# Optimization experiments

Measured on AMD Instinct MI355X. Metric: run time of the kernel, lower is better.

Reference implementation:

```python
import math
import jax, jax.numpy as jnp
import numpy as np

B, C, H, W = 8, 128, 128, 128

def _cosine_basis(n):
    pos = (jnp.arange(n, dtype=jnp.float32) + 0.5) / n          # [n]
    freq = jnp.arange(n, dtype=jnp.float32)[:, None]            # [n,1]
    basis = jnp.cos(freq * pos[None, :] * math.pi) * math.sqrt(2.0 / n)
    return basis.at[0, :].multiply(1.0 / math.sqrt(2.0))        # [n,n]


def setup_inputs() -> dict:
    key = jax.random.key(0)
    ks = jax.random.split(key, 12)
    s = 0.02
    return {
        "x":        jax.random.normal(ks[0], (B, C, H, W), jnp.float32),
        "dw_w":     jax.random.normal(ks[1], (C, 1, 3, 3), jnp.float32) * s,
        "dw_b":     jnp.zeros((C,), jnp.float32),
        "in_w":     jax.random.normal(ks[2], (2 * C, C), jnp.float32) * s,
        "in_b":     jnp.zeros((2 * C,), jnp.float32),
        "out_w":    jax.random.normal(ks[3], (C, C), jnp.float32) * s,
        "out_b":    jnp.zeros((C,), jnp.float32),
        "ln_w":     jnp.ones((C,), jnp.float32),
        "ln_b":     jnp.zeros((C,), jnp.float32),
        "ph_w":     jax.random.normal(ks[4], (C, C), jnp.float32) * s,
        "ph_b":     jnp.zeros((C,), jnp.float32),
        "wave_speed": jnp.ones((1,), jnp.float32),
        "damping":    jnp.full((1,), 0.1, jnp.float32),
        "freq_embed": jax.random.normal(ks[5], (H, W, C), jnp.float32) * s,
    }


def reference(x, dw_w, dw_b, in_w, in_b, out_w, out_b, ln_w, ln_b,
              ph_w, ph_b, wave_speed, damping, freq_embed):
    # depthwise 3x3 conv (groups=C), padding=1
    mixed = jax.lax.conv_general_dilated(
        x, dw_w, window_strides=(1, 1), padding=((1, 1), (1, 1)),
        dimension_numbers=("NCHW", "OIHW", "NCHW"), feature_group_count=C)
    mixed = mixed + dw_b[None, :, None, None]
    mixed = jnp.transpose(mixed, (0, 2, 3, 1))                  # [B,H,W,C]

    proj = mixed @ in_w.T + in_b                                # [B,H,W,2C]
    carrier, gate = jnp.split(proj, 2, axis=-1)

    cos_h = _cosine_basis(H)
    cos_w = _cosine_basis(W)
    # DCT-II along H then W
    spectral = jnp.einsum("bhwc,nh->bnwc", carrier, cos_h)
    spectral = jnp.einsum("bnwc,mw->bnmc", spectral, cos_w)     # [B,H,W,C] (freq)

    # phase modulation (base_resolution == H == W, so no resize)
    phase = jax.nn.gelu(freq_embed @ ph_w.T + ph_b, approximate=False)  # [H,W,C]
    wave_phase = wave_speed * phase                             # broadcast [H,W,C]
    vel_scale = jnp.sin(wave_phase) / jnp.maximum(jnp.abs(wave_speed), 1e-6)
    modulated = (jnp.cos(wave_phase) + vel_scale * (1.0 + 0.5 * damping)) * spectral

    # inverse DCT
    fused = jnp.einsum("bnmc,wm->bnwc", modulated, cos_w.T)
    fused = jnp.einsum("bnwc,hn->bhwc", fused, cos_h.T)         # [B,H,W,C]

    # LayerNorm over channels
    mu = jnp.mean(fused, axis=-1, keepdims=True)
    var = jnp.mean(jnp.square(fused - mu), axis=-1, keepdims=True)
    fused = (fused - mu) / jnp.sqrt(var + 1e-5) * ln_w + ln_b

    fused = fused * jax.nn.silu(gate)
    out = fused @ out_w.T + out_b                               # [B,H,W,C]
    return jnp.transpose(out, (0, 3, 1, 2))                     # [B,C,H,W]
```

## Files before the change

### kernel.cpp

```cpp
#include <hip/hip_runtime.h>
#include <math.h>

#ifndef M_PI
#define M_PI 3.14159265358979323846
#endif

typedef float fx4 __attribute__((ext_vector_type(4)));
typedef __bf16 bf16x8 __attribute__((ext_vector_type(8)));
typedef __bf16 bf16x4 __attribute__((ext_vector_type(4)));

__device__ __forceinline__ unsigned short f2bf(float f){
  union { float f; unsigned u; } v; v.f = f;
  unsigned r = v.u + 0x7FFFu + ((v.u >> 16) & 1u);
  return (unsigned short)(r >> 16);
}
__device__ __forceinline__ float bf2f(unsigned short u){
  union { unsigned u; float f; } v; v.u = ((unsigned)u) << 16;
  return v.f;
}
__device__ __forceinline__ int swz(int row, int colbyte){
  return row*256 + (colbyte ^ ((row & 7) << 4));
}

template<typename FA, typename FB>
__device__ __forceinline__ void run_gemm(FA la, FB lb, fx4 (&acc)[4][4]){
  bf16x8 a[2][4], b[2][4];
  #pragma unroll
  for (int mi=0;mi<4;mi++){ a[0][mi]=la(mi,0); b[0][mi]=lb(mi,0); }
  #pragma unroll
  for (int ks=0; ks<4; ks++){
    int cur = ks&1, nxt = cur^1;
    if (ks<3){
      #pragma unroll
      for (int mi=0;mi<4;mi++){ a[nxt][mi]=la(mi,ks+1); b[nxt][mi]=lb(mi,ks+1); }
    }
    #pragma unroll
    for (int mi=0;mi<4;mi++)
      #pragma unroll
      for (int ni=0;ni<4;ni++)
        acc[mi][ni] = __builtin_amdgcn_mfma_f32_16x16x32_bf16(a[cur][mi], b[cur][ni], acc[mi][ni], 0, 0, 0);
  }
}

template<typename FA0, typename FA1, typename FB>
__device__ __forceinline__ void run_pair_sharedB(FA0 la0, FA1 la1, FB lb,
                                                 fx4 (&acc0)[4][4], fx4 (&acc1)[4][4]){
  bf16x8 a0[2][4], a1[2][4], b[2][4];
  #pragma unroll
  for (int mi=0;mi<4;mi++){ a0[0][mi]=la0(mi,0); a1[0][mi]=la1(mi,0); b[0][mi]=lb(mi,0); }
  #pragma unroll
  for (int ks=0; ks<4; ks++){
    int cur = ks&1, nxt = cur^1;
    if (ks<3){
      #pragma unroll
      for (int mi=0;mi<4;mi++){ a0[nxt][mi]=la0(mi,ks+1); a1[nxt][mi]=la1(mi,ks+1); b[nxt][mi]=lb(mi,ks+1); }
    }
    #pragma unroll
    for (int mi=0;mi<4;mi++)
      #pragma unroll
      for (int ni=0;ni<4;ni++){
        acc0[mi][ni] = __builtin_amdgcn_mfma_f32_16x16x32_bf16(a0[cur][mi], b[cur][ni], acc0[mi][ni], 0, 0, 0);
        acc1[mi][ni] = __builtin_amdgcn_mfma_f32_16x16x32_bf16(a1[cur][mi], b[cur][ni], acc1[mi][ni], 0, 0, 0);
      }
  }
}

template<typename FA, typename FB0, typename FB1>
__device__ __forceinline__ void run_pair_sharedA(FA la, FB0 lb0, FB1 lb1,
                                                 fx4 (&acc0)[4][4], fx4 (&acc1)[4][4]){
  bf16x8 a[2][4], b0[2][4], b1[2][4];
  #pragma unroll
  for (int mi=0;mi<4;mi++){ a[0][mi]=la(mi,0); b0[0][mi]=lb0(mi,0); b1[0][mi]=lb1(mi,0); }
  #pragma unroll
  for (int ks=0; ks<4; ks++){
    int cur = ks&1, nxt = cur^1;
    if (ks<3){
      #pragma unroll
      for (int mi=0;mi<4;mi++){ a[nxt][mi]=la(mi,ks+1); b0[nxt][mi]=lb0(mi,ks+1); b1[nxt][mi]=lb1(mi,ks+1); }
    }
    #pragma unroll
    for (int mi=0;mi<4;mi++)
      #pragma unroll
      for (int ni=0;ni<4;ni++){
        acc0[mi][ni] = __builtin_amdgcn_mfma_f32_16x16x32_bf16(a[cur][mi], b0[cur][ni], acc0[mi][ni], 0, 0, 0);
        acc1[mi][ni] = __builtin_amdgcn_mfma_f32_16x16x32_bf16(a[cur][mi], b1[cur][ni], acc1[mi][ni], 0, 0, 0);
      }
  }
}

__global__ __launch_bounds__(256) void k1_prep_cast_conv(
    const float* __restrict__ in_w, const float* __restrict__ ph_w,
    const float* __restrict__ out_w, const float* __restrict__ fe,
    const float* __restrict__ x, const float* __restrict__ dw_w,
    const float* __restrict__ dw_b,
    unsigned short* __restrict__ basis_bf, unsigned short* __restrict__ basisT_bf,
    unsigned short* __restrict__ ph_w_bf, unsigned short* __restrict__ in_w_bf,
    unsigned short* __restrict__ out_w_bf, unsigned short* __restrict__ feb,
    unsigned short* __restrict__ conv)
{
  int blk = blockIdx.x;
  int t = threadIdx.x;
  if (blk < 128){
    if (t >= 128) return;
    int n = blk, h = t;
    double arg = (double)(n*(2*h+1)) * (M_PI/256.0);
    double v = cos(arg) * 0.125;
    if (n==0) v *= 0.7071067811865476;
    unsigned short bv = f2bf((float)v);
    basis_bf[n*128+h]  = bv;
    basisT_bf[h*128+n] = bv;
    ph_w_bf[n*128+h]  = f2bf(ph_w[n*128+h]);
    in_w_bf[n*128+h]        = f2bf(in_w[n*128+h]);
    in_w_bf[(n+128)*128+h]  = f2bf(in_w[(n+128)*128+h]);
    out_w_bf[n*128+h]       = f2bf(out_w[n*128+h]);
    return;
  }
  if (blk < 1152){
    int idx = (blk-128)*256 + t;
    const float* s = fe + (size_t)idx*8;
    float4 f0 = *(const float4*)s;
    float4 f1 = *(const float4*)(s+4);
    unsigned short o[8];
    o[0]=f2bf(f0.x); o[1]=f2bf(f0.y); o[2]=f2bf(f0.z); o[3]=f2bf(f0.w);
    o[4]=f2bf(f1.x); o[5]=f2bf(f1.y); o[6]=f2bf(f1.z); o[7]=f2bf(f1.w);
    *(int4*)(feb + (size_t)idx*8) = *(const int4*)o;
    return;
  }
  {
    int bb = blk - 1152;
    int plane = bb >> 2, band = bb & 3;
    int c = plane & 127;
    const float* xp = x + (size_t)plane*16384;
    unsigned short* op = conv + (size_t)plane*16384;
    const float* kw = dw_w + c*9;
    float k0=kw[0],k1=kw[1],k2=kw[2],k3=kw[3],k4=kw[4],k5=kw[5],k6=kw[6],k7=kw[7],k8=kw[8];
    float bias = dw_b[c];
    int q = t & 31;
    int w0 = q*4;
    int rg = t >> 5;
    int h0 = band*32 + rg*4;
    bool le = (q==0), re = (q==31);
    float4 fA, fB, fC; float lA,rA,lB,rB,lC,rC;
    #define LOADROW(hh, f, l, r) { \
      int hc = (hh)<0 ? 0 : ((hh)>127 ? 127 : (hh)); \
      f = *(const float4*)(xp + hc*128 + w0); \
      float lu = __shfl_up(f.w, 1, 32); \
      float rd = __shfl_down(f.x, 1, 32); \
      l = le ? 0.f : lu; \
      r = re ? 0.f : rd; \
      if ((hh)<0 || (hh)>127){ f = make_float4(0.f,0.f,0.f,0.f); l=0.f; r=0.f; } \
    }
    LOADROW(h0-1, fA,lA,rA);
    LOADROW(h0,   fB,lB,rB);
    #pragma unroll
    for (int i=0;i<4;i++){
      LOADROW(h0+1+i, fC,lC,rC);
      float4 o;
      o.x = bias; o.y = bias; o.z = bias; o.w = bias;
      o.x = fmaf(k0,lA,  fmaf(k1,fA.x, fmaf(k2,fA.y, o.x)));
      o.y = fmaf(k0,fA.x,fmaf(k1,fA.y, fmaf(k2,fA.z, o.y)));
      o.z = fmaf(k0,fA.y,fmaf(k1,fA.z, fmaf(k2,fA.w, o.z)));
      o.w = fmaf(k0,fA.z,fmaf(k1,fA.w, fmaf(k2,rA,   o.w)));
      o.x = fmaf(k3,lB,  fmaf(k4,fB.x, fmaf(k5,fB.y, o.x)));
      o.y = fmaf(k3,fB.x,fmaf(k4,fB.y, fmaf(k5,fB.z, o.y)));
      o.z = fmaf(k3,fB.y,fmaf(k4,fB.z, fmaf(k5,fB.w, o.z)));
      o.w = fmaf(k3,fB.z,fmaf(k4,fB.w, fmaf(k5,rB,   o.w)));
      o.x = fmaf(k6,lC,  fmaf(k7,fC.x, fmaf(k8,fC.y, o.x)));
      o.y = fmaf(k6,fC.x,fmaf(k7,fC.y, fmaf(k8,fC.z, o.y)));
      o.z = fmaf(k6,fC.y,fmaf(k7,fC.z, fmaf(k8,fC.w, o.z)));
      o.w = fmaf(k6,fC.z,fmaf(k7,fC.w, fmaf(k8,rC,   o.w)));
      bf16x4 v;
      v[0]=(__bf16)o.x; v[1]=(__bf16)o.y; v[2]=(__bf16)o.z; v[3]=(__bf16)o.w;
      *(bf16x4*)(op + (size_t)(h0+i)*128 + w0) = v;
      fA=fB; lA=lB; rA=rB;
      fB=fC; lB=lC; rB=rC;
    }
    #undef LOADROW
  }
}

__global__ __launch_bounds__(512) void k2_inproj_projk(
  const unsigned short* __restrict__ conv, const unsigned short* __restrict__ in_w_bf,
  const float* __restrict__ in_b, unsigned short* __restrict__ carrier,
  unsigned short* __restrict__ gate,
  const unsigned short* __restrict__ feb, const unsigned short* __restrict__ ph_w_bf,
  float* __restrict__ projT)
{
  int blk = blockIdx.x;
  int t = threadIdx.x;
  if (blk >= 1024){
    if (t >= 256) return;
    int r0 = (blk - 1024) * 128;
    int l = t & 63, wid = t >> 6;
    int wm = wid >> 1, wn = wid & 1;
    int lr = l & 15, lk = (l>>4)*8, ld4 = (l>>4)*4;
    fx4 acc[4][4];
    #pragma unroll
    for (int i=0;i<4;i++) for (int j=0;j<4;j++) acc[i][j] = (fx4){0.f,0.f,0.f,0.f};
    run_gemm(
      [&](int mi,int ks)->bf16x8{ return *(const bf16x8*)(feb + (size_t)(r0 + wm*64+mi*16+lr)*128 + ks*32+lk); },
      [&](int ni,int ks)->bf16x8{ return *(const bf16x8*)(ph_w_bf + (size_t)(wn*64+ni*16+lr)*128 + ks*32+lk); },
      acc);
    #pragma unroll
    for (int mi=0;mi<4;mi++)
      #pragma unroll
      for (int ni=0;ni<4;ni++){
        int c = wn*64 + ni*16 + lr;
        int r = r0 + wm*64 + mi*16 + ld4;
        *(fx4*)(projT + (size_t)c*16384 + r) = acc[mi][ni];
      }
    return;
  }
  __shared__ char A[32768];
  int b = blk>>7, h = blk&127;
  const unsigned short* C = conv + (size_t)b*2097152 + h*128;
  {
    int wl = t & 63, grp = t >> 6;
    #pragma unroll
    for (int p=0;p<2;p++){
      int w = wl + 64*p;
      #pragma unroll
      for (int q=0;q<4;q++){
        int c0 = (q*8 + grp)*4;
        ushort4 v;
        v.x = C[(size_t)(c0+0)*16384 + w];
        v.y = C[(size_t)(c0+1)*16384 + w];
        v.z = C[(size_t)(c0+2)*16384 + w];
        v.w = C[(size_t)(c0+3)*16384 + w];
        *(ushort4*)(A + swz(w, c0*2)) = v;
      }
    }
  }
  __syncthreads();
  int l = t & 63, wid = t >> 6;
  int wm = wid >> 2, wn = wid & 3;
  int lr = l & 15, lk = (l>>4)*8, ld4 = (l>>4)*4;
  fx4 acc[4][4];
  #pragma unroll
  for (int i=0;i<4;i++) for (int j=0;j<4;j++) acc[i][j] = (fx4){0.f,0.f,0.f,0.f};
  run_gemm(
    [&](int mi,int ks)->bf16x8{ return *(const bf16x8*)(A + swz(wm*64+mi*16+lr, (ks*32+lk)*2)); },
    [&](int ni,int ks)->bf16x8{ return *(const bf16x8*)(in_w_bf + (size_t)(wn*64+ni*16+lr)*128 + ks*32+lk); },
    acc);
  __syncthreads();
  if (wn < 2){
    #pragma unroll
    for (int mi=0;mi<4;mi++)
      #pragma unroll
      for (int ni=0;ni<4;ni++){
        int n = wn*64 + ni*16 + lr;
        int w0 = wm*64 + mi*16 + ld4;
        float bias = in_b[n];
        ushort4 v;
        v.x=f2bf(acc[mi][ni][0]+bias); v.y=f2bf(acc[mi][ni][1]+bias);
        v.z=f2bf(acc[mi][ni][2]+bias); v.w=f2bf(acc[mi][ni][3]+bias);
        *(ushort4*)(carrier + (size_t)(b*128+n)*16384 + h*128 + w0) = v;
      }
  } else {
    #pragma unroll
    for (int mi=0;mi<4;mi++)
      #pragma unroll
      for (int ni=0;ni<4;ni++){
        int n = wn*64 + ni*16 + lr;
        int c = n - 128;
        int w0 = wm*64 + mi*16 + ld4;
        float bias = in_b[n];
        #pragma unroll
        for (int r=0;r<4;r++){
          float v = acc[mi][ni][r] + bias;
          float s = v / (1.0f + __expf(-v));
          *(unsigned short*)(A + swz(w0+r, c*2)) = f2bf(s);
        }
      }
  }
  __syncthreads();
  {
    unsigned short* gout = gate + ((size_t)(b*128+h))*16384;
    int w = t >> 2, cq = (t & 3) * 32;
    #pragma unroll
    for (int i=0;i<4;i++){
      int c0 = cq + i*8;
      int4 v = *(const int4*)(A + swz(w, c0*2));
      *(int4*)(gout + w*128 + c0) = v;
    }
  }
}

__global__ __launch_bounds__(256) void modfin_kernel(
  const float* __restrict__ projT, const float* __restrict__ ph_b,
  const float* __restrict__ wave_speed, const float* __restrict__ damping,
  float* __restrict__ modT)
{
  int blk = blockIdx.x;
  int c = blk >> 4, qb = blk & 15;
  int t = threadIdx.x;
  int q = qb*8 + (t>>5);
  int p0 = (t & 31)*4;
  float ws0 = wave_speed[0];
  float dmp = damping[0];
  float inv = 1.0f / fmaxf(fabsf(ws0), 1e-6f);
  float dampf = 1.0f + 0.5f*dmp;
  float bc = ph_b[c];
  const float* src = projT + (size_t)c*16384 + q;
  float o[4];
  #pragma unroll
  for (int i=0;i<4;i++){
    float v = src[(size_t)(p0+i)*128] + bc;
    float g = 0.5f*v*(1.0f + erff(v*0.70710678118f));
    float wp = ws0*g;
    o[i] = __cosf(wp) + __sinf(wp)*inv*dampf;
  }
  *(float4*)(modT + ((size_t)c*128 + q)*128 + p0) = make_float4(o[0],o[1],o[2],o[3]);
}

__global__ __launch_bounds__(256) void wave_kernel(
  const unsigned short* __restrict__ carrier,
  const unsigned short* __restrict__ basis,
  const unsigned short* __restrict__ basisT,
  const float* __restrict__ modT,
  unsigned short* __restrict__ fused)
{
  __shared__ char U0[32768];
  __shared__ char U1[32768];
  int blk = blockIdx.x;
  int c = blk & 127;
  const unsigned short* X0 = carrier + (size_t)blk*16384;
  const unsigned short* X1 = carrier + (size_t)(blk+512)*16384;
  unsigned short* F0 = fused + (size_t)blk*16384;
  unsigned short* F1 = fused + (size_t)(blk+512)*16384;
  int t = threadIdx.x;
  int l = t & 63, wid = t >> 6;
  int wm = wid >> 1, wn = wid & 1;
  int lr = l & 15, lk = (l>>4)*8, ld4 = (l>>4)*4;
  fx4 acc0[4][4], acc1[4][4];

  #define ZACC { _Pragma("unroll") for (int i=0;i<4;i++) _Pragma("unroll") for (int j=0;j<4;j++){ acc0[i][j]=(fx4){0.f,0.f,0.f,0.f}; acc1[i][j]=(fx4){0.f,0.f,0.f,0.f}; } }
  #define TSTORE(BUF0, BUF1) { \
    _Pragma("unroll") for (int mi=0;mi<4;mi++) \
      _Pragma("unroll") for (int ni=0;ni<4;ni++){ \
        int rr = wn*64 + ni*16 + lr, cc = wm*64 + mi*16 + ld4; \
        bf16x4 v0, v1; \
        v0[0]=(__bf16)acc0[mi][ni][0]; v0[1]=(__bf16)acc0[mi][ni][1]; \
        v0[2]=(__bf16)acc0[mi][ni][2]; v0[3]=(__bf16)acc0[mi][ni][3]; \
        v1[0]=(__bf16)acc1[mi][ni][0]; v1[1]=(__bf16)acc1[mi][ni][1]; \
        v1[2]=(__bf16)acc1[mi][ni][2]; v1[3]=(__bf16)acc1[mi][ni][3]; \
        *(bf16x4*)(BUF0 + swz(rr, cc*2)) = v0; \
        *(bf16x4*)(BUF1 + swz(rr, cc*2)) = v1; \
      } }

  ZACC;
  run_pair_sharedB(
    [&](int mi,int ks)->bf16x8{ return *(const bf16x8*)(X0 + (size_t)(wm*64+mi*16+lr)*128 + ks*32+lk); },
    [&](int mi,int ks)->bf16x8{ return *(const bf16x8*)(X1 + (size_t)(wm*64+mi*16+lr)*128 + ks*32+lk); },
    [&](int ni,int ks)->bf16x8{ return *(const bf16x8*)(basis + (size_t)(wn*64+ni*16+lr)*128 + ks*32+lk); },
    acc0, acc1);
  TSTORE(U0, U1);
  __syncthreads();

  ZACC;
  run_pair_sharedA(
    [&](int mi,int ks)->bf16x8{ return *(const bf16x8*)(basis + (size_t)(wm*64+mi*16+lr)*128 + ks*32+lk); },
    [&](int ni,int ks)->bf16x8{ return *(const bf16x8*)(U0 + swz(wn*64+ni*16+lr, (ks*32+lk)*2)); },
    [&](int ni,int ks)->bf16x8{ return *(const bf16x8*)(U1 + swz(wn*64+ni*16+lr, (ks*32+lk)*2)); },
    acc0, acc1);
  {
    const float* Mc = modT + (size_t)c*16384;
    #pragma unroll
    for (int mi=0;mi<4;mi++)
      #pragma unroll
      for (int ni=0;ni<4;ni++){
        int n0 = wm*64 + mi*16 + ld4, m = wn*64 + ni*16 + lr;
        fx4 mv = *(const fx4*)(Mc + (size_t)m*128 + n0);
        acc0[mi][ni] *= mv;
        acc1[mi][ni] *= mv;
      }
  }
  __syncthreads();
  TSTORE(U0, U1);
  __syncthreads();

  ZACC;
  run_pair_sharedB(
    [&](int mi,int ks)->bf16x8{ return *(const bf16x8*)(U0 + swz(wm*64+mi*16+lr, (ks*32+lk)*2)); },
    [&](int mi,int ks)->bf16x8{ return *(const bf16x8*)(U1 + swz(wm*64+mi*16+lr, (ks*32+lk)*2)); },
    [&](int ni,int ks)->bf16x8{ return *(const bf16x8*)(basisT + (size_t)(wn*64+ni*16+lr)*128 + ks*32+lk); },
    acc0, acc1);
  __syncthreads();
  TSTORE(U0, U1);
  __syncthreads();

  ZACC;
  run_pair_sharedA(
    [&](int mi,int ks)->bf16x8{ return *(const bf16x8*)(basisT + (size_t)(wm*64+mi*16+lr)*128 + ks*32+lk); },
    [&](int ni,int ks)->bf16x8{ return *(const bf16x8*)(U0 + swz(wn*64+ni*16+lr, (ks*32+lk)*2)); },
    [&](int ni,int ks)->bf16x8{ return *(const bf16x8*)(U1 + swz(wn*64+ni*16+lr, (ks*32+lk)*2)); },
    acc0, acc1);
  #pragma unroll
  for (int mi=0;mi<4;mi++)
    #pragma unroll
    for (int ni=0;ni<4;ni++){
      int hh = wn*64 + ni*16 + lr, w0 = wm*64 + mi*16 + ld4;
      bf16x4 v0, v1;
      v0[0]=(__bf16)acc0[mi][ni][0]; v0[1]=(__bf16)acc0[mi][ni][1];
      v0[2]=(__bf16)acc0[mi][ni][2]; v0[3]=(__bf16)acc0[mi][ni][3];
      v1[0]=(__bf16)acc1[mi][ni][0]; v1[1]=(__bf16)acc1[mi][ni][1];
      v1[2]=(__bf16)acc1[mi][ni][2]; v1[3]=(__bf16)acc1[mi][ni][3];
      *(bf16x4*)(F0 + hh*128 + w0) = v0;
      *(bf16x4*)(F1 + hh*128 + w0) = v1;
    }
  #undef ZACC
  #undef TSTORE
}

__global__ __launch_bounds__(256) void final_kernel(
  const unsigned short* __restrict__ fused, const unsigned short* __restrict__ gate,
  const unsigned short* __restrict__ out_w_bf, const float* __restrict__ out_b,
  const float* __restrict__ ln_w, const float* __restrict__ ln_b,
  float* __restrict__ out)
{
  __shared__ char Fl[32768];
  __shared__ char Al[32768];
  __shared__ float red[256], red2[256];
  __shared__ float mu[128], rs[128];
  int blk = blockIdx.x; int b = blk>>7, h = blk&127;
  const unsigned short* Fsrc = fused + (size_t)b*2097152 + h*128;
  const unsigned short* G = gate + (size_t)blk*16384;
  int t = threadIdx.x;
  {
    int c = t>>1, wq = (t&1)*64;
    #pragma unroll
    for (int i=0;i<8;i++){
      int w0 = wq + i*8;
      int4 v = *(const int4*)(Fsrc + (size_t)c*16384 + w0);
      *(int4*)(Fl + swz(c, w0*2)) = v;
    }
  }
  __syncthreads();
  {
    int w = t&127, half = t>>7;
    float s=0.f, q=0.f;
    for (int i=0;i<64;i++){
      int c = half*64 + i;
      float f = bf2f(*(const unsigned short*)(Fl + swz(c, w*2)));
      s += f; q = fmaf(f,f,q);
    }
    red[t]=s; red2[t]=q;
  }
  __syncthreads();
  if (t < 128){
    float ss = red[t]+red[t+128], qq = red2[t]+red2[t+128];
    float m = ss*(1.f/128.f);
    float var = qq*(1.f/128.f) - m*m;
    mu[t]=m; rs[t]=rsqrtf(var+1e-5f);
  }
  __syncthreads();
  {
    int w = t>>1, cq = (t&1)*64;
    float m_ = mu[w], r_ = rs[w];
    #pragma unroll
    for (int i=0;i<8;i++){
      int c0 = cq + i*8;
      ushort4 g0 = *(const ushort4*)(G + (size_t)w*128 + c0);
      ushort4 g1 = *(const ushort4*)(G + (size_t)w*128 + c0 + 4);
      unsigned short ov[8];
      unsigned short gv[8] = {g0.x,g0.y,g0.z,g0.w,g1.x,g1.y,g1.z,g1.w};
      #pragma unroll
      for (int j=0;j<8;j++){
        int cc = c0+j;
        float f = bf2f(*(const unsigned short*)(Fl + swz(cc, w*2)));
        float a = fmaf((f-m_)*r_, ln_w[cc], ln_b[cc]) * bf2f(gv[j]);
        ov[j] = f2bf(a);
      }
      *(int4*)(Al + swz(w, c0*2)) = *(const int4*)ov;
    }
  }
  __syncthreads();
  int l = t & 63, wid = t >> 6;
  int wm = wid >> 1, wn = wid & 1;
  int lr = l & 15, lk = (l>>4)*8, ld4 = (l>>4)*4;
  fx4 acc[4][4];
  #pragma unroll
  for (int i=0;i<4;i++) for (int j=0;j<4;j++) acc[i][j] = (fx4){0.f,0.f,0.f,0.f};
  run_gemm(
    [&](int mi,int ks)->bf16x8{ return *(const bf16x8*)(Al + swz(wm*64+mi*16+lr, (ks*32+lk)*2)); },
    [&](int ni,int ks)->bf16x8{ return *(const bf16x8*)(out_w_bf + (size_t)(wn*64+ni*16+lr)*128 + ks*32+lk); },
    acc);
  #pragma unroll
  for (int mi=0;mi<4;mi++)
    #pragma unroll
    for (int ni=0;ni<4;ni++){
      int j = wn*64 + ni*16 + lr, w0 = wm*64 + mi*16 + ld4;
      float bj = out_b[j];
      fx4 o = acc[mi][ni];
      o[0]+=bj; o[1]+=bj; o[2]+=bj; o[3]+=bj;
      *(fx4*)(out + ((size_t)(b*128 + j)*128 + h)*128 + w0) = o;
    }
}

extern "C" void kernel_launch(void* const* d_in, const int* in_sizes, int n_in,
                              void* d_out, int out_size, void* d_ws, size_t ws_size,
                              hipStream_t stream)
{
  const float* x      = (const float*)d_in[0];
  const float* dw_w   = (const float*)d_in[1];
  const float* dw_b   = (const float*)d_in[2];
  const float* in_w   = (const float*)d_in[3];
  const float* in_b   = (const float*)d_in[4];
  const float* out_w  = (const float*)d_in[5];
  const float* out_b  = (const float*)d_in[6];
  const float* ln_w   = (const float*)d_in[7];
  const float* ln_b   = (const float*)d_in[8];
  const float* ph_w   = (const float*)d_in[9];
  const float* ph_b   = (const float*)d_in[10];
  const float* wsp    = (const float*)d_in[11];
  const float* dmp    = (const float*)d_in[12];
  const float* fe     = (const float*)d_in[13];
  float* outp = (float*)d_out;

  float* modT  = (float*)d_ws;
  float* projT = modT + 2097152;
  unsigned short* feb      = (unsigned short*)(projT + 2097152);
  unsigned short* conv     = feb     + 2097152;
  unsigned short* carrier  = conv    + 16777216;
  unsigned short* gate     = carrier + 16777216;
  unsigned short* fusedb   = gate    + 16777216;
  unsigned short* basis_bf = fusedb  + 16777216;
  unsigned short* basisT_bf= basis_bf + 16384;
  unsigned short* in_w_bf  = basisT_bf + 16384;
  unsigned short* out_w_bf = in_w_bf + 32768;
  unsigned short* ph_w_bf  = out_w_bf + 16384;

  k1_prep_cast_conv<<<5248,256,0,stream>>>(in_w, ph_w, out_w, fe, x, dw_w, dw_b,
      basis_bf, basisT_bf, ph_w_bf, in_w_bf, out_w_bf, feb, conv);
  k2_inproj_projk<<<1152,512,0,stream>>>(conv, in_w_bf, in_b, carrier, gate,
      feb, ph_w_bf, projT);
  modfin_kernel<<<2048,256,0,stream>>>(projT, ph_b, wsp, dmp, modT);
  wave_kernel<<<512,256,0,stream>>>(carrier, basis_bf, basisT_bf, modT, fusedb);
  final_kernel<<<1024,256,0,stream>>>(fusedb, gate, out_w_bf, out_b, ln_w, ln_b, outp);
}
```

Baseline: 156.3 us.

## Fuse depthwise conv into in-projection kernel, drop conv intermediate buffer

Moves the depthwise 3x3 convolution from the prep kernel into the in-projection GEMM kernel, computing each (b,h) row's conv output directly into shared memory. This removes the bf16 conv intermediate write and its strided re-read from global memory. In exchange each block reads three input rows per channel (halo redundancy across blocks) and uses more registers per thread, with scattered 2-byte LDS stores.

```diff
diff --git a/kernel.cpp b/kernel.cpp
--- a/kernel.cpp
+++ b/kernel.cpp
@@ -88,15 +88,12 @@
   }
 }
 
-__global__ __launch_bounds__(256) void k1_prep_cast_conv(
+__global__ __launch_bounds__(256) void k1_prep_cast(
     const float* __restrict__ in_w, const float* __restrict__ ph_w,
     const float* __restrict__ out_w, const float* __restrict__ fe,
-    const float* __restrict__ x, const float* __restrict__ dw_w,
-    const float* __restrict__ dw_b,
     unsigned short* __restrict__ basis_bf, unsigned short* __restrict__ basisT_bf,
     unsigned short* __restrict__ ph_w_bf, unsigned short* __restrict__ in_w_bf,
-    unsigned short* __restrict__ out_w_bf, unsigned short* __restrict__ feb,
-    unsigned short* __restrict__ conv)
+    unsigned short* __restrict__ out_w_bf, unsigned short* __restrict__ feb)
 {
   int blk = blockIdx.x;
   int t = threadIdx.x;
@@ -115,7 +112,7 @@
     out_w_bf[n*128+h]       = f2bf(out_w[n*128+h]);
     return;
   }
-  if (blk < 1152){
+  {
     int idx = (blk-128)*256 + t;
     const float* s = fe + (size_t)idx*8;
     float4 f0 = *(const float4*)s;
@@ -124,63 +121,13 @@
     o[0]=f2bf(f0.x); o[1]=f2bf(f0.y); o[2]=f2bf(f0.z); o[3]=f2bf(f0.w);
     o[4]=f2bf(f1.x); o[5]=f2bf(f1.y); o[6]=f2bf(f1.z); o[7]=f2bf(f1.w);
     *(int4*)(feb + (size_t)idx*8) = *(const int4*)o;
-    return;
-  }
-  {
-    int bb = blk - 1152;
-    int plane = bb >> 2, band = bb & 3;
-    int c = plane & 127;
-    const float* xp = x + (size_t)plane*16384;
-    unsigned short* op = conv + (size_t)plane*16384;
-    const float* kw = dw_w + c*9;
-    float k0=kw[0],k1=kw[1],k2=kw[2],k3=kw[3],k4=kw[4],k5=kw[5],k6=kw[6],k7=kw[7],k8=kw[8];
-    float bias = dw_b[c];
-    int q = t & 31;
-    int w0 = q*4;
-    int rg = t >> 5;
-    int h0 = band*32 + rg*4;
-    bool le = (q==0), re = (q==31);
-    float4 fA, fB, fC; float lA,rA,lB,rB,lC,rC;
-    #define LOADROW(hh, f, l, r) { \
-      int hc = (hh)<0 ? 0 : ((hh)>127 ? 127 : (hh)); \
-      f = *(const float4*)(xp + hc*128 + w0); \
-      float lu = __shfl_up(f.w, 1, 32); \
-      float rd = __shfl_down(f.x, 1, 32); \
-      l = le ? 0.f : lu; \
-      r = re ? 0.f : rd; \
-      if ((hh)<0 || (hh)>127){ f = make_float4(0.f,0.f,0.f,0.f); l=0.f; r=0.f; } \
-    }
-    LOADROW(h0-1, fA,lA,rA);
-    LOADROW(h0,   fB,lB,rB);
-    #pragma unroll
-    for (int i=0;i<4;i++){
-      LOADROW(h0+1+i, fC,lC,rC);
-      float4 o;
-      o.x = bias; o.y = bias; o.z = bias; o.w = bias;
-      o.x = fmaf(k0,lA,  fmaf(k1,fA.x, fmaf(k2,fA.y, o.x)));
-      o.y = fmaf(k0,fA.x,fmaf(k1,fA.y, fmaf(k2,fA.z, o.y)));
-      o.z = fmaf(k0,fA.y,fmaf(k1,fA.z, fmaf(k2,fA.w, o.z)));
-      o.w = fmaf(k0,fA.z,fmaf(k1,fA.w, fmaf(k2,rA,   o.w)));
-      o.x = fmaf(k3,lB,  fmaf(k4,fB.x, fmaf(k5,fB.y, o.x)));
-      o.y = fmaf(k3,fB.x,fmaf(k4,fB.y, fmaf(k5,fB.z, o.y)));
-      o.z = fmaf(k3,fB.y,fmaf(k4,fB.z, fmaf(k5,fB.w, o.z)));
-      o.w = fmaf(k3,fB.z,fmaf(k4,fB.w, fmaf(k5,rB,   o.w)));
-      o.x = fmaf(k6,lC,  fmaf(k7,fC.x, fmaf(k8,fC.y, o.x)));
-      o.y = fmaf(k6,fC.x,fmaf(k7,fC.y, fmaf(k8,fC.z, o.y)));
-      o.z = fmaf(k6,fC.y,fmaf(k7,fC.z, fmaf(k8,fC.w, o.z)));
-      o.w = fmaf(k6,fC.z,fmaf(k7,fC.w, fmaf(k8,rC,   o.w)));
-      bf16x4 v;
-      v[0]=(__bf16)o.x; v[1]=(__bf16)o.y; v[2]=(__bf16)o.z; v[3]=(__bf16)o.w;
-      *(bf16x4*)(op + (size_t)(h0+i)*128 + w0) = v;
-      fA=fB; lA=lB; rA=rB;
-      fB=fC; lB=lC; rB=rC;
-    }
-    #undef LOADROW
-  }
-}
-
-__global__ __launch_bounds__(512) void k2_inproj_projk(
-  const unsigned short* __restrict__ conv, const unsigned short* __restrict__ in_w_bf,
+  }
+}
+
+__global__ __launch_bounds__(512) void k2_convinproj_projk(
+  const float* __restrict__ x, const float* __restrict__ dw_w,
+  const float* __restrict__ dw_b,
+  const unsigned short* __restrict__ in_w_bf,
   const float* __restrict__ in_b, unsigned short* __restrict__ carrier,
   unsigned short* __restrict__ gate,
   const unsigned short* __restrict__ feb, const unsigned short* __restrict__ ph_w_bf,
@@ -213,23 +160,40 @@
   }
   __shared__ char A[32768];
   int b = blk>>7, h = blk&127;
-  const unsigned short* C = conv + (size_t)b*2097152 + h*128;
-  {
-    int wl = t & 63, grp = t >> 6;
-    #pragma unroll
-    for (int p=0;p<2;p++){
-      int w = wl + 64*p;
-      #pragma unroll
-      for (int q=0;q<4;q++){
-        int c0 = (q*8 + grp)*4;
-        ushort4 v;
-        v.x = C[(size_t)(c0+0)*16384 + w];
-        v.y = C[(size_t)(c0+1)*16384 + w];
-        v.z = C[(size_t)(c0+2)*16384 + w];
-        v.w = C[(size_t)(c0+3)*16384 + w];
-        *(ushort4*)(A + swz(w, c0*2)) = v;
-      }
-    }
+  {
+    int c = t >> 2, wq = (t & 3) * 32;
+    const float* xc = x + ((size_t)(b*128 + c))*16384;
+    const float* kw = dw_w + c*9;
+    float kv[9];
+    #pragma unroll
+    for (int i=0;i<9;i++) kv[i] = kw[i];
+    float bias = dw_b[c];
+    float out[32];
+    #pragma unroll
+    for (int i=0;i<32;i++) out[i] = bias;
+    #pragma unroll
+    for (int dy=0; dy<3; dy++){
+      int hh = h + dy - 1;
+      if (hh < 0 || hh > 127) continue;
+      const float* r = xc + hh*128 + wq;
+      float v[32];
+      #pragma unroll
+      for (int i=0;i<8;i++){
+        float4 f = *(const float4*)(r + i*4);
+        v[i*4+0]=f.x; v[i*4+1]=f.y; v[i*4+2]=f.z; v[i*4+3]=f.w;
+      }
+      float lft = (wq > 0)    ? r[-1] : 0.f;
+      float rgt = (wq < 96)   ? r[32] : 0.f;
+      float ka = kv[dy*3], kb = kv[dy*3+1], kc = kv[dy*3+2];
+      out[0] = fmaf(ka, lft, fmaf(kb, v[0], fmaf(kc, v[1], out[0])));
+      #pragma unroll
+      for (int i=1;i<31;i++)
+        out[i] = fmaf(ka, v[i-1], fmaf(kb, v[i], fmaf(kc, v[i+1], out[i])));
+      out[31] = fmaf(ka, v[30], fmaf(kb, v[31], fmaf(kc, rgt, out[31])));
+    }
+    #pragma unroll
+    for (int i=0;i<32;i++)
+      *(unsigned short*)(A + swz(wq+i, c*2)) = f2bf(out[i]);
   }
   __syncthreads();
   int l = t & 63, wid = t >> 6;
@@ -520,8 +484,7 @@
   float* modT  = (float*)d_ws;
   float* projT = modT + 2097152;
   unsigned short* feb      = (unsigned short*)(projT + 2097152);
-  unsigned short* conv     = feb     + 2097152;
-  unsigned short* carrier  = conv    + 16777216;
+  unsigned short* carrier  = feb     + 2097152;
   unsigned short* gate     = carrier + 16777216;
   unsigned short* fusedb   = gate    + 16777216;
   unsigned short* basis_bf = fusedb  + 16777216;
@@ -530,10 +493,10 @@
   unsigned short* out_w_bf = in_w_bf + 32768;
   unsigned short* ph_w_bf  = out_w_bf + 16384;
 
-  k1_prep_cast_conv<<<5248,256,0,stream>>>(in_w, ph_w, out_w, fe, x, dw_w, dw_b,
-      basis_bf, basisT_bf, ph_w_bf, in_w_bf, out_w_bf, feb, conv);
-  k2_inproj_projk<<<1152,512,0,stream>>>(conv, in_w_bf, in_b, carrier, gate,
-      feb, ph_w_bf, projT);
+  k1_prep_cast<<<1152,256,0,stream>>>(in_w, ph_w, out_w, fe,
+      basis_bf, basisT_bf, ph_w_bf, in_w_bf, out_w_bf, feb);
+  k2_convinproj_projk<<<1152,512,0,stream>>>(x, dw_w, dw_b, in_w_bf, in_b,
+      carrier, gate, feb, ph_w_bf, projT);
   modfin_kernel<<<2048,256,0,stream>>>(projT, ph_b, wsp, dmp, modT);
   wave_kernel<<<512,256,0,stream>>>(carrier, basis_bf, basisT_bf, modT, fusedb);
   final_kernel<<<1024,256,0,stream>>>(fusedb, gate, out_w_bf, out_b, ln_w, ln_b, outp);
```

After: 191.6 us. 22.6% more time.

## Process two H rows per block in final kernel sharing out_w fragments

Applied to the files above, without the earlier changes.

The final LayerNorm+gate+out-projection kernel now handles two adjacent h rows per block (512 blocks instead of 1024), loading both fused tiles, computing two sets of LN statistics, and running a paired GEMM that reuses the out_w B fragments across both rows. The gated activations are staged in registers and written back over the fused LDS buffers, which frees the separate A buffer. The aim is to halve global reads of out_w per output, improve write contiguity to neighbouring h rows, and amortise per-block overhead. In exchange, each thread holds two 64-element register arrays plus two accumulator sets, which raises register pressure and risks spills and lower occupancy, and the grid shrinks to 512 blocks.

```diff
diff --git a/kernel.cpp b/kernel.cpp
--- a/kernel.cpp
+++ b/kernel.cpp
@@ -418,82 +418,116 @@
   const float* __restrict__ ln_w, const float* __restrict__ ln_b,
   float* __restrict__ out)
 {
-  __shared__ char Fl[32768];
-  __shared__ char Al[32768];
+  __shared__ char Fl0[32768];
+  __shared__ char Fl1[32768];
   __shared__ float red[256], red2[256];
-  __shared__ float mu[128], rs[128];
-  int blk = blockIdx.x; int b = blk>>7, h = blk&127;
-  const unsigned short* Fsrc = fused + (size_t)b*2097152 + h*128;
-  const unsigned short* G = gate + (size_t)blk*16384;
+  __shared__ float mu[2][128], rs[2][128];
+  int blk = blockIdx.x;
+  int b = blk>>6, hp = blk&63;
+  int h0 = hp*2, h1 = h0+1;
+  const unsigned short* Fs0 = fused + (size_t)b*2097152 + h0*128;
+  const unsigned short* Fs1 = Fs0 + 128;
+  const unsigned short* G0 = gate + ((size_t)(b*128+h0))*16384;
+  const unsigned short* G1 = G0 + 16384;
   int t = threadIdx.x;
   {
     int c = t>>1, wq = (t&1)*64;
     #pragma unroll
     for (int i=0;i<8;i++){
       int w0 = wq + i*8;
-      int4 v = *(const int4*)(Fsrc + (size_t)c*16384 + w0);
-      *(int4*)(Fl + swz(c, w0*2)) = v;
+      *(int4*)(Fl0 + swz(c, w0*2)) = *(const int4*)(Fs0 + (size_t)c*16384 + w0);
+      *(int4*)(Fl1 + swz(c, w0*2)) = *(const int4*)(Fs1 + (size_t)c*16384 + w0);
     }
   }
   __syncthreads();
   {
     int w = t&127, half = t>>7;
-    float s=0.f, q=0.f;
+    float s0=0.f,q0=0.f,s1=0.f,q1=0.f;
     for (int i=0;i<64;i++){
       int c = half*64 + i;
-      float f = bf2f(*(const unsigned short*)(Fl + swz(c, w*2)));
-      s += f; q = fmaf(f,f,q);
-    }
-    red[t]=s; red2[t]=q;
-  }
-  __syncthreads();
-  if (t < 128){
-    float ss = red[t]+red[t+128], qq = red2[t]+red2[t+128];
-    float m = ss*(1.f/128.f);
-    float var = qq*(1.f/128.f) - m*m;
-    mu[t]=m; rs[t]=rsqrtf(var+1e-5f);
-  }
-  __syncthreads();
+      float f0 = bf2f(*(const unsigned short*)(Fl0 + swz(c, w*2)));
+      float f1 = bf2f(*(const unsigned short*)(Fl1 + swz(c, w*2)));
+      s0 += f0; q0 = fmaf(f0,f0,q0);
+      s1 += f1; q1 = fmaf(f1,f1,q1);
+    }
+    red[t]=s0; red2[t]=q0;
+    __syncthreads();
+    if (half==0){
+      float ss=red[w]+red[w+128], qq=red2[w]+red2[w+128];
+      float m = ss*(1.f/128.f);
+      float var = qq*(1.f/128.f) - m*m;
+      mu[0][w]=m; rs[0][w]=rsqrtf(var+1e-5f);
+    }
+    __syncthreads();
+    red[t]=s1; red2[t]=q1;
+    __syncthreads();
+    if (half==0){
+      float ss=red[w]+red[w+128], qq=red2[w]+red2[w+128];
+      float m = ss*(1.f/128.f);
+      float var = qq*(1.f/128.f) - m*m;
+      mu[1][w]=m; rs[1][w]=rsqrtf(var+1e-5f);
+    }
+  }
+  __syncthreads();
+  unsigned short a0[64], a1[64];
   {
     int w = t>>1, cq = (t&1)*64;
-    float m_ = mu[w], r_ = rs[w];
+    float m0=mu[0][w], r0=rs[0][w], m1=mu[1][w], r1=rs[1][w];
     #pragma unroll
     for (int i=0;i<8;i++){
       int c0 = cq + i*8;
-      ushort4 g0 = *(const ushort4*)(G + (size_t)w*128 + c0);
-      ushort4 g1 = *(const ushort4*)(G + (size_t)w*128 + c0 + 4);
-      unsigned short ov[8];
-      unsigned short gv[8] = {g0.x,g0.y,g0.z,g0.w,g1.x,g1.y,g1.z,g1.w};
+      ushort4 ga = *(const ushort4*)(G0 + (size_t)w*128 + c0);
+      ushort4 gb = *(const ushort4*)(G0 + (size_t)w*128 + c0 + 4);
+      ushort4 gc = *(const ushort4*)(G1 + (size_t)w*128 + c0);
+      ushort4 gd = *(const ushort4*)(G1 + (size_t)w*128 + c0 + 4);
+      unsigned short gv0[8] = {ga.x,ga.y,ga.z,ga.w,gb.x,gb.y,gb.z,gb.w};
+      unsigned short gv1[8] = {gc.x,gc.y,gc.z,gc.w,gd.x,gd.y,gd.z,gd.w};
       #pragma unroll
       for (int j=0;j<8;j++){
         int cc = c0+j;
-        float f = bf2f(*(const unsigned short*)(Fl + swz(cc, w*2)));
-        float a = fmaf((f-m_)*r_, ln_w[cc], ln_b[cc]) * bf2f(gv[j]);
-        ov[j] = f2bf(a);
-      }
-      *(int4*)(Al + swz(w, c0*2)) = *(const int4*)ov;
+        float lw = ln_w[cc], lb = ln_b[cc];
+        float f0 = bf2f(*(const unsigned short*)(Fl0 + swz(cc, w*2)));
+        float f1 = bf2f(*(const unsigned short*)(Fl1 + swz(cc, w*2)));
+        a0[i*8+j] = f2bf(fmaf((f0-m0)*r0, lw, lb) * bf2f(gv0[j]));
+        a1[i*8+j] = f2bf(fmaf((f1-m1)*r1, lw, lb) * bf2f(gv1[j]));
+      }
+    }
+  }
+  __syncthreads();
+  {
+    int w = t>>1, cq = (t&1)*64;
+    #pragma unroll
+    for (int i=0;i<8;i++){
+      int c0 = cq + i*8;
+      *(int4*)(Fl0 + swz(w, c0*2)) = *(const int4*)&a0[i*8];
+      *(int4*)(Fl1 + swz(w, c0*2)) = *(const int4*)&a1[i*8];
     }
   }
   __syncthreads();
   int l = t & 63, wid = t >> 6;
   int wm = wid >> 1, wn = wid & 1;
   int lr = l & 15, lk = (l>>4)*8, ld4 = (l>>4)*4;
-  fx4 acc[4][4];
-  #pragma unroll
-  for (int i=0;i<4;i++) for (int j=0;j<4;j++) acc[i][j] = (fx4){0.f,0.f,0.f,0.f};
-  run_gemm(
-    [&](int mi,int ks)->bf16x8{ return *(const bf16x8*)(Al + swz(wm*64+mi*16+lr, (ks*32+lk)*2)); },
+  fx4 acc0[4][4], acc1[4][4];
+  #pragma unroll
+  for (int i=0;i<4;i++) for (int j=0;j<4;j++){ acc0[i][j]=(fx4){0.f,0.f,0.f,0.f}; acc1[i][j]=(fx4){0.f,0.f,0.f,0.f}; }
+  run_pair_sharedB(
+    [&](int mi,int ks)->bf16x8{ return *(const bf16x8*)(Fl0 + swz(wm*64+mi*16+lr, (ks*32+lk)*2)); },
+    [&](int mi,int ks)->bf16x8{ return *(const bf16x8*)(Fl1 + swz(wm*64+mi*16+lr, (ks*32+lk)*2)); },
     [&](int ni,int ks)->bf16x8{ return *(const bf16x8*)(out_w_bf + (size_t)(wn*64+ni*16+lr)*128 + ks*32+lk); },
-    acc);
+    acc0, acc1);
   #pragma unroll
   for (int mi=0;mi<4;mi++)
     #pragma unroll
     for (int ni=0;ni<4;ni++){
       int j = wn*64 + ni*16 + lr, w0 = wm*64 + mi*16 + ld4;
       float bj = out_b[j];
-      fx4 o = acc[mi][ni];
-      o[0]+=bj; o[1]+=bj; o[2]+=bj; o[3]+=bj;
-      *(fx4*)(out + ((size_t)(b*128 + j)*128 + h)*128 + w0) = o;
+      fx4 o0 = acc0[mi][ni];
+      fx4 o1 = acc1[mi][ni];
+      o0[0]+=bj; o0[1]+=bj; o0[2]+=bj; o0[3]+=bj;
+      o1[0]+=bj; o1[1]+=bj; o1[2]+=bj; o1[3]+=bj;
+      float* base = out + ((size_t)(b*128 + j)*128)*128 + w0;
+      *(fx4*)(base + (size_t)h0*128) = o0;
+      *(fx4*)(base + (size_t)h1*128) = o1;
     }
 }
 
@@ -536,5 +570,5 @@
       feb, ph_w_bf, projT);
   modfin_kernel<<<2048,256,0,stream>>>(projT, ph_b, wsp, dmp, modT);
   wave_kernel<<<512,256,0,stream>>>(carrier, basis_bf, basisT_bf, modT, fusedb);
-  final_kernel<<<1024,256,0,stream>>>(fusedb, gate, out_w_bf, out_b, ln_w, ln_b, outp);
-}
+  final_kernel<<<512,256,0,stream>>>(fusedb, gate, out_w_bf, out_b, ln_w, ln_b, outp);
+}
```

Result: no change. 159.4 us (+1.9%).
